# Optimization experiments

Measured on AMD Instinct MI355X. Metric: run time of the kernel, lower is better.

## Reference

```python
import jax, jax.numpy as jnp
import numpy as np

P = 50          # num_predicates
E = 2000        # num_entities
M = 64          # max_facts_per_query
F = 2_000_000   # num facts
N = 500_000     # num queries
BASE = E + 2    # pack base = max(constant_no, padding_idx) + 2


def setup_inputs() -> dict:
    key = jax.random.key(0)
    k1, k2, k3, k4, k5, k6 = jax.random.split(key, 6)
    fp = jax.random.randint(k1, (F,), 0, P, dtype=jnp.int32)
    fs = jax.random.randint(k2, (F,), 0, E, dtype=jnp.int32)
    fo = jax.random.randint(k3, (F,), 0, E, dtype=jnp.int32)
    facts_idx = jnp.stack([fp, fs, fo], axis=1)  # [F, 3]
    preds = jax.random.randint(k4, (N,), 0, P, dtype=jnp.int32)
    bound_args = jax.random.randint(k5, (N,), 0, E, dtype=jnp.int32)
    direction = jax.random.randint(k6, (N,), 0, 2, dtype=jnp.int32)
    return {"facts_idx": facts_idx, "preds": preds,
            "bound_args": bound_args, "direction": direction}


def _build_csr(keys, vals, num_buckets):
    """Sort vals by key; build offset table via scatter-add + cumsum (as in torch)."""
    order = jnp.argsort(keys)               # stable sort, matches pre-hash-sorted facts
    sorted_vals = vals[order]
    counts = jnp.zeros(num_buckets + 1, dtype=jnp.int32).at[keys + 1].add(1)
    offsets = jnp.cumsum(counts)
    return sorted_vals, offsets


def reference(facts_idx, preds, bound_args, direction):
    # --- _FactIndexBase: sort facts by packed 64-bit hash (lexicographic p,s,o) ---
    fp, fs, fo = facts_idx[:, 0], facts_idx[:, 1], facts_idx[:, 2]
    hashes = (fp * BASE + fs) * BASE + fo   # fits int32 for these dims
    h_order = jnp.argsort(hashes)
    fp, fs, fo = fp[h_order], fs[h_order], fo[h_order]

    # --- _build_inverted_indices: (pred,subj)->objs and (pred,obj)->subjs CSR ---
    ps_sorted_objs, ps_offsets = _build_csr(fp * E + fs, fo, P * E)
    po_sorted_subjs, po_offsets = _build_csr(fp * E + fo, fs, P * E)

    # --- enumerate() ---
    keys = preds * E + bound_args                               # [N]
    starts_ps = ps_offsets[keys]
    counts_ps = jnp.clip(ps_offsets[keys + 1] - starts_ps, 0, M)
    starts_po = po_offsets[keys]
    counts_po = jnp.clip(po_offsets[keys + 1] - starts_po, 0, M)
    is_obj = direction == 0                                     # [N] bool
    starts = jnp.where(is_obj, starts_ps, starts_po)
    counts = jnp.where(is_obj, counts_ps, counts_po)

    pos = jnp.arange(M, dtype=jnp.int32)[None, :]               # [1, M]
    valid = pos < counts[:, None]                               # [N, M]
    size = ps_sorted_objs.shape[0]                              # == F for both arrays
    gi = jnp.clip(starts[:, None] + pos, 0, size - 1)           # [N, M]
    vals_obj = ps_sorted_objs[gi]
    vals_subj = po_sorted_subjs[gi]
    candidates = jnp.where(is_obj[:, None], vals_obj, vals_subj)
    return candidates, valid
```

## Files before the change

### kernel.cpp

```cpp
#include <hip/hip_runtime.h>

#define PCONST 50
#define ECONST 2000
#define MCONST 64
#define NKEY   (PCONST * ECONST)
#define KPB    256
#define NBIN   ((NKEY + KPB - 1) / KPB)
#define NBIN2  (2 * NBIN)
#define SC_THREADS 1024
#define SC_CHUNK   8192
#define FPT    (SC_CHUNK / SC_THREADS)
#define CAP    6144

typedef int ivec4 __attribute__((ext_vector_type(4)));
typedef ivec4 ivec4_a4 __attribute__((aligned(4)));

__global__ void __launch_bounds__(SC_THREADS)
scatter_sort(const int* __restrict__ facts,
             int* __restrict__ bincur,
             unsigned* __restrict__ slab, int F) {
    __shared__ unsigned ordered[2 * SC_CHUNK];
    __shared__ int cnt[NBIN2];
    __shared__ int lbase[NBIN2];
    __shared__ int cur[NBIN2];
    __shared__ int base[NBIN2];
    __shared__ int wsum[16];

    int t = threadIdx.x;
    int blockStart = blockIdx.x * SC_CHUNK;
    int n = min(SC_CHUNK, F - blockStart);
    if (n <= 0) return;

    for (int i = t; i < NBIN2; i += SC_THREADS) cnt[i] = 0;
    __syncthreads();

    int myBase = blockStart + t * FPT;
    int myN = F - myBase;
    myN = (myN < 0) ? 0 : ((myN > FPT) ? FPT : myN);

    unsigned vps[FPT], vpo[FPT];

    if (myN == FPT) {
        const int4* p = (const int4*)(facts + 3 * myBase);
        int4 w0 = p[0], w1 = p[1], w2 = p[2], w3 = p[3], w4 = p[4], w5 = p[5];
        int kps, kpo;
        kps = w0.x * ECONST + w0.y; kpo = w0.x * ECONST + w0.z;
        vps[0] = ((unsigned)kps << 11) | (unsigned)w0.z;
        vpo[0] = ((unsigned)kpo << 11) | (unsigned)w0.y;
        atomicAdd(&cnt[kps >> 8], 1); atomicAdd(&cnt[NBIN + (kpo >> 8)], 1);
        kps = w0.w * ECONST + w1.x; kpo = w0.w * ECONST + w1.y;
        vps[1] = ((unsigned)kps << 11) | (unsigned)w1.y;
        vpo[1] = ((unsigned)kpo << 11) | (unsigned)w1.x;
        atomicAdd(&cnt[kps >> 8], 1); atomicAdd(&cnt[NBIN + (kpo >> 8)], 1);
        kps = w1.z * ECONST + w1.w; kpo = w1.z * ECONST + w2.x;
        vps[2] = ((unsigned)kps << 11) | (unsigned)w2.x;
        vpo[2] = ((unsigned)kpo << 11) | (unsigned)w1.w;
        atomicAdd(&cnt[kps >> 8], 1); atomicAdd(&cnt[NBIN + (kpo >> 8)], 1);
        kps = w2.y * ECONST + w2.z; kpo = w2.y * ECONST + w2.w;
        vps[3] = ((unsigned)kps << 11) | (unsigned)w2.w;
        vpo[3] = ((unsigned)kpo << 11) | (unsigned)w2.z;
        atomicAdd(&cnt[kps >> 8], 1); atomicAdd(&cnt[NBIN + (kpo >> 8)], 1);
        kps = w3.x * ECONST + w3.y; kpo = w3.x * ECONST + w3.z;
        vps[4] = ((unsigned)kps << 11) | (unsigned)w3.z;
        vpo[4] = ((unsigned)kpo << 11) | (unsigned)w3.y;
        atomicAdd(&cnt[kps >> 8], 1); atomicAdd(&cnt[NBIN + (kpo >> 8)], 1);
        kps = w3.w * ECONST + w4.x; kpo = w3.w * ECONST + w4.y;
        vps[5] = ((unsigned)kps << 11) | (unsigned)w4.y;
        vpo[5] = ((unsigned)kpo << 11) | (unsigned)w4.x;
        atomicAdd(&cnt[kps >> 8], 1); atomicAdd(&cnt[NBIN + (kpo >> 8)], 1);
        kps = w4.z * ECONST + w4.w; kpo = w4.z * ECONST + w5.x;
        vps[6] = ((unsigned)kps << 11) | (unsigned)w5.x;
        vpo[6] = ((unsigned)kpo << 11) | (unsigned)w4.w;
        atomicAdd(&cnt[kps >> 8], 1); atomicAdd(&cnt[NBIN + (kpo >> 8)], 1);
        kps = w5.y * ECONST + w5.z; kpo = w5.y * ECONST + w5.w;
        vps[7] = ((unsigned)kps << 11) | (unsigned)w5.w;
        vpo[7] = ((unsigned)kpo << 11) | (unsigned)w5.z;
        atomicAdd(&cnt[kps >> 8], 1); atomicAdd(&cnt[NBIN + (kpo >> 8)], 1);
    } else {
        for (int i = 0; i < myN; ++i) {
            int g = myBase + i;
            int fp = facts[3 * g], fs = facts[3 * g + 1], fo = facts[3 * g + 2];
            int kps = fp * ECONST + fs;
            int kpo = fp * ECONST + fo;
            vps[i] = ((unsigned)kps << 11) | (unsigned)fo;
            vpo[i] = ((unsigned)kpo << 11) | (unsigned)fs;
            atomicAdd(&cnt[kps >> 8], 1);
            atomicAdd(&cnt[NBIN + (kpo >> 8)], 1);
        }
    }
    __syncthreads();

    {
        int lane = t & 63, w = t >> 6;
        int c = (t < NBIN2) ? cnt[t] : 0;
        int inc = c;
        for (int d = 1; d < 64; d <<= 1) {
            int v = __shfl_up(inc, d);
            if (lane >= d) inc += v;
        }
        if (lane == 63) wsum[w] = inc;
        __syncthreads();
        if (t < NBIN2) {
            int wbase = 0;
            for (int i = 0; i < w; ++i) wbase += wsum[i];
            int excl = wbase + inc - c;
            lbase[t] = excl;
            cur[t]   = excl;
        }
    }
    __syncthreads();
    for (int i = t; i < NBIN2; i += SC_THREADS) {
        int c = cnt[i];
        base[i] = c ? atomicAdd(&bincur[i], c) : 0;
    }
    __syncthreads();

    #pragma unroll
    for (int i = 0; i < FPT; ++i) {
        if (i >= myN) break;
        unsigned ps = vps[i];
        int pos = atomicAdd(&cur[ps >> 19], 1);
        ordered[pos] = ps;
        unsigned po = vpo[i];
        pos = atomicAdd(&cur[NBIN + (po >> 19)], 1);
        ordered[pos] = (1u << 28) | po;
    }
    __syncthreads();

    int n2 = 2 * n;
    for (int j = t; j < n2; j += SC_THREADS) {
        unsigned v = ordered[j];
        int cbin = (int)((v >> 19) & 511u) + ((v >> 28) ? NBIN : 0);
        int pos  = base[cbin] + (j - lbase[cbin]);
        if (pos < CAP) slab[(size_t)cbin * CAP + pos] = v & 0x0FFFFFFFu;
    }
}

__global__ void binsort_kernel(const int* __restrict__ bincur,
                               const unsigned* __restrict__ slab,
                               int* __restrict__ off_ps,
                               int* __restrict__ off_po,
                               int* __restrict__ data_ps,
                               int* __restrict__ data_po, int F) {
    __shared__ unsigned buf[CAP];
    __shared__ unsigned short outv[CAP];
    __shared__ int hist[KPB];
    __shared__ int wsum[4];
    __shared__ int red[4];

    int wg = blockIdx.x;
    int* offout;
    int* data;
    const int* curbase;
    int b;
    if (wg < NBIN) { offout = off_ps; data = data_ps; curbase = bincur;        b = wg; }
    else           { offout = off_po; data = data_po; curbase = bincur + NBIN; b = wg - NBIN; }
    int t = threadIdx.x;
    int lane = t & 63, w = t >> 6;

    int s = 0;
    for (int i = t; i < b; i += KPB) s += curbase[i];
    for (int d = 1; d < 64; d <<= 1) s += __shfl_xor(s, d);
    if (lane == 0) red[w] = s;
    __syncthreads();
    int start = red[0] + red[1] + red[2] + red[3];

    int key0 = b * KPB;
    int len  = min(curbase[b], CAP);
    const unsigned* src = slab + (size_t)wg * CAP;

    if (t == 0 && b == 0) offout[NKEY] = F;

    for (int i = t; i < len; i += KPB) buf[i] = src[i];
    hist[t] = 0;
    __syncthreads();
    for (int i = t; i < len; i += KPB)
        atomicAdd(&hist[(int)(buf[i] >> 11) - key0], 1);
    __syncthreads();

    int c = hist[t];
    int inc = c;
    for (int d = 1; d < 64; d <<= 1) {
        int v = __shfl_up(inc, d);
        if (lane >= d) inc += v;
    }
    if (lane == 63) wsum[w] = inc;
    __syncthreads();
    int wbase = 0;
    for (int i = 0; i < w; ++i) wbase += wsum[i];
    int excl = wbase + inc - c;
    int gk = key0 + t;
    if (gk < NKEY) offout[gk] = start + excl;
    __syncthreads();
    hist[t] = excl;
    __syncthreads();

    for (int i = t; i < len; i += KPB) {
        unsigned v = buf[i];
        int lk  = (int)(v >> 11) - key0;
        int pos = atomicAdd(&hist[lk], 1);
        outv[pos] = (unsigned short)(v & 2047u);
    }
    __syncthreads();

    {
        int s0 = (t == 0) ? 0 : hist[t - 1];
        int e0 = hist[t];
        for (int i = s0 + 1; i < e0; ++i) {
            unsigned short v = outv[i]; int j = i - 1;
            while (j >= s0 && outv[j] > v) { outv[j + 1] = outv[j]; --j; }
            outv[j + 1] = v;
        }
    }
    __syncthreads();

    for (int i = t; i < len; i += KPB) data[start + i] = (int)outv[i];

    if ((wg == NBIN - 1 || wg == NBIN2 - 1) && t < 64 && len > 0)
        data[F + t] = (int)outv[len - 1];
}

__global__ void query_kernel(const int* __restrict__ preds,
                             const int* __restrict__ bound,
                             const int* __restrict__ dir,
                             const int* __restrict__ off_ps,
                             const int* __restrict__ off_po,
                             const int* __restrict__ vals_ps,
                             const int* __restrict__ vals_po,
                             int* __restrict__ cand,
                             int* __restrict__ valid, int N, int F) {
    int gwave  = (blockIdx.x * blockDim.x + threadIdx.x) >> 6;
    int lane   = threadIdx.x & 63;
    int nwaves = (gridDim.x * blockDim.x) >> 6;
    int grp = lane >> 4;
    int sl  = (lane & 15) * 4;

    for (int qb = gwave * 64; qb < N; qb += nwaves * 64) {
        int q = qb + lane;
        unsigned pk = 0;
        if (q < N) {
            int key = preds[q] * ECONST + bound[q];
            int dd  = dir[q];
            const int* off = (dd == 0) ? off_ps : off_po;
            int s0 = off[key];
            int c0 = min(off[key + 1] - s0, MCONST);
            if (c0 < 0) c0 = 0;
            pk = ((unsigned)s0 << 9) | ((unsigned)(dd != 0) << 8) | (unsigned)c0;
        }
        int nq = min(64, N - qb);
        for (int j4 = 0; j4 < nq; j4 += 4) {
            int j = j4 + grp;
            unsigned pj = (unsigned)__shfl((int)pk, j);
            if (j < nq) {
                int c  = (int)(pj & 255u);
                int s  = (int)(pj >> 9);
                const int* vals = (pj & 256u) ? vals_po : vals_ps;
                ivec4 cv = *(const ivec4_a4*)(vals + s + sl);
                ivec4 vv;
                vv.x = (sl     < c) ? 1 : 0;
                vv.y = (sl + 1 < c) ? 1 : 0;
                vv.z = (sl + 2 < c) ? 1 : 0;
                vv.w = (sl + 3 < c) ? 1 : 0;
                size_t o = (size_t)(qb + j) * MCONST + sl;
                __builtin_nontemporal_store(cv, (ivec4*)&cand[o]);
                __builtin_nontemporal_store(vv, (ivec4*)&valid[o]);
            }
        }
    }
}

extern "C" void kernel_launch(void* const* d_in, const int* in_sizes, int n_in,
                              void* d_out, int out_size, void* d_ws, size_t ws_size,
                              hipStream_t stream) {
    const int* facts = (const int*)d_in[0];
    const int* preds = (const int*)d_in[1];
    const int* bound = (const int*)d_in[2];
    const int* dir   = (const int*)d_in[3];
    int F = in_sizes[0] / 3;
    int N = in_sizes[1];

    int* ws       = (int*)d_ws;
    int* off_ps   = ws;
    int* off_po   = off_ps + NKEY + 4;
    int* bincur   = off_po + NKEY + 4;
    int* pad      = bincur + NBIN2;
    size_t ofs = (size_t)(pad - ws);
    ofs = (ofs + 3) & ~(size_t)3;
    int* data_ps = ws + ofs;
    int* data_po = data_ps + F + 64;
    unsigned* slab = (unsigned*)(data_po + F + 64);

    hipMemsetAsync(bincur, 0, (size_t)NBIN2 * sizeof(int), stream);

    int nChunks = (F + SC_CHUNK - 1) / SC_CHUNK;
    scatter_sort<<<nChunks, SC_THREADS, 0, stream>>>(facts, bincur, slab, F);
    binsort_kernel<<<NBIN2, KPB, 0, stream>>>(bincur, slab,
                                              off_ps, off_po, data_ps, data_po, F);

    int* cand  = (int*)d_out;
    int* valid = cand + (size_t)N * MCONST;
    int qBlocks = (N / 64 + 3) / 4 + 1;
    query_kernel<<<qBlocks, 256, 0, stream>>>(
        preds, bound, dir, off_ps, off_po, data_ps, data_po, cand, valid, N, F);
}
```

Measured before the change: 161.9 us.

## Pack start/count into one query table and store CSR values as 16-bit

The binsort kernel now writes a single packed table entry per key, holding the start offset shifted left 7 bits and the count clamped to 64. It no longer writes separate offset arrays for the two CSRs. Both CSR value arrays go into one shared ushort buffer, which halves the footprint of the gathered candidates. Each query then needs one table load instead of two offset loads, and reads 2-byte values. The cost is four scalar ushort loads per lane in place of one vector load. The packing assumes start offsets fit in 25 bits, which holds for 2F+64 at these sizes.

```diff
diff --git a/kernel.cpp b/kernel.cpp
--- a/kernel.cpp
+++ b/kernel.cpp
@@ -13,7 +13,6 @@
 #define CAP    6144
 
 typedef int ivec4 __attribute__((ext_vector_type(4)));
-typedef ivec4 ivec4_a4 __attribute__((aligned(4)));
 
 __global__ void __launch_bounds__(SC_THREADS)
 scatter_sort(const int* __restrict__ facts,
@@ -138,10 +137,9 @@
 
 __global__ void binsort_kernel(const int* __restrict__ bincur,
                                const unsigned* __restrict__ slab,
-                               int* __restrict__ off_ps,
-                               int* __restrict__ off_po,
-                               int* __restrict__ data_ps,
-                               int* __restrict__ data_po, int F) {
+                               unsigned* __restrict__ qtab,
+                               unsigned short* __restrict__ dataA,
+                               int F) {
     __shared__ unsigned buf[CAP];
     __shared__ unsigned short outv[CAP];
     __shared__ int hist[KPB];
@@ -149,12 +147,10 @@
     __shared__ int red[4];
 
     int wg = blockIdx.x;
-    int* offout;
-    int* data;
-    const int* curbase;
-    int b;
-    if (wg < NBIN) { offout = off_ps; data = data_ps; curbase = bincur;        b = wg; }
-    else           { offout = off_po; data = data_po; curbase = bincur + NBIN; b = wg - NBIN; }
+    int csr = (wg < NBIN) ? 0 : 1;
+    int b   = wg - csr * NBIN;
+    const int* curbase = bincur + csr * NBIN;
+    int gofs = csr ? (F + 64) : 0;
     int t = threadIdx.x;
     int lane = t & 63, w = t >> 6;
 
@@ -168,8 +164,6 @@
     int key0 = b * KPB;
     int len  = min(curbase[b], CAP);
     const unsigned* src = slab + (size_t)wg * CAP;
-
-    if (t == 0 && b == 0) offout[NKEY] = F;
 
     for (int i = t; i < len; i += KPB) buf[i] = src[i];
     hist[t] = 0;
@@ -190,7 +184,9 @@
     for (int i = 0; i < w; ++i) wbase += wsum[i];
     int excl = wbase + inc - c;
     int gk = key0 + t;
-    if (gk < NKEY) offout[gk] = start + excl;
+    if (gk < NKEY)
+        qtab[csr * NKEY + gk] =
+            ((unsigned)(gofs + start + excl) << 7) | (unsigned)min(c, MCONST);
     __syncthreads();
     hist[t] = excl;
     __syncthreads();
@@ -214,21 +210,19 @@
     }
     __syncthreads();
 
-    for (int i = t; i < len; i += KPB) data[start + i] = (int)outv[i];
+    for (int i = t; i < len; i += KPB) dataA[gofs + start + i] = outv[i];
 
     if ((wg == NBIN - 1 || wg == NBIN2 - 1) && t < 64 && len > 0)
-        data[F + t] = (int)outv[len - 1];
+        dataA[gofs + F + t] = outv[len - 1];
 }
 
 __global__ void query_kernel(const int* __restrict__ preds,
                              const int* __restrict__ bound,
                              const int* __restrict__ dir,
-                             const int* __restrict__ off_ps,
-                             const int* __restrict__ off_po,
-                             const int* __restrict__ vals_ps,
-                             const int* __restrict__ vals_po,
+                             const unsigned* __restrict__ qtab,
+                             const unsigned short* __restrict__ dataA,
                              int* __restrict__ cand,
-                             int* __restrict__ valid, int N, int F) {
+                             int* __restrict__ valid, int N) {
     int gwave  = (blockIdx.x * blockDim.x + threadIdx.x) >> 6;
     int lane   = threadIdx.x & 63;
     int nwaves = (gridDim.x * blockDim.x) >> 6;
@@ -239,24 +233,21 @@
         int q = qb + lane;
         unsigned pk = 0;
         if (q < N) {
-            int key = preds[q] * ECONST + bound[q];
-            int dd  = dir[q];
-            const int* off = (dd == 0) ? off_ps : off_po;
-            int s0 = off[key];
-            int c0 = min(off[key + 1] - s0, MCONST);
-            if (c0 < 0) c0 = 0;
-            pk = ((unsigned)s0 << 9) | ((unsigned)(dd != 0) << 8) | (unsigned)c0;
+            int idx = ((dir[q] != 0) ? NKEY : 0) + preds[q] * ECONST + bound[q];
+            pk = qtab[idx];
         }
         int nq = min(64, N - qb);
         for (int j4 = 0; j4 < nq; j4 += 4) {
             int j = j4 + grp;
             unsigned pj = (unsigned)__shfl((int)pk, j);
             if (j < nq) {
-                int c  = (int)(pj & 255u);
-                int s  = (int)(pj >> 9);
-                const int* vals = (pj & 256u) ? vals_po : vals_ps;
-                ivec4 cv = *(const ivec4_a4*)(vals + s + sl);
-                ivec4 vv;
+                int c = (int)(pj & 127u);
+                int s = (int)(pj >> 7);
+                ivec4 cv, vv;
+                cv.x = (int)dataA[s + sl];
+                cv.y = (int)dataA[s + sl + 1];
+                cv.z = (int)dataA[s + sl + 2];
+                cv.w = (int)dataA[s + sl + 3];
                 vv.x = (sl     < c) ? 1 : 0;
                 vv.y = (sl + 1 < c) ? 1 : 0;
                 vv.z = (sl + 2 < c) ? 1 : 0;
@@ -279,27 +270,24 @@
     int F = in_sizes[0] / 3;
     int N = in_sizes[1];
 
-    int* ws       = (int*)d_ws;
-    int* off_ps   = ws;
-    int* off_po   = off_ps + NKEY + 4;
-    int* bincur   = off_po + NKEY + 4;
-    int* pad      = bincur + NBIN2;
+    int* ws        = (int*)d_ws;
+    unsigned* qtab = (unsigned*)ws;
+    int* bincur    = ws + 2 * NKEY;
+    int* pad       = bincur + NBIN2;
     size_t ofs = (size_t)(pad - ws);
     ofs = (ofs + 3) & ~(size_t)3;
-    int* data_ps = ws + ofs;
-    int* data_po = data_ps + F + 64;
-    unsigned* slab = (unsigned*)(data_po + F + 64);
+    unsigned short* dataA = (unsigned short*)(ws + ofs);
+    unsigned* slab = (unsigned*)(dataA + 2 * (size_t)F + 128);
 
     hipMemsetAsync(bincur, 0, (size_t)NBIN2 * sizeof(int), stream);
 
     int nChunks = (F + SC_CHUNK - 1) / SC_CHUNK;
     scatter_sort<<<nChunks, SC_THREADS, 0, stream>>>(facts, bincur, slab, F);
-    binsort_kernel<<<NBIN2, KPB, 0, stream>>>(bincur, slab,
-                                              off_ps, off_po, data_ps, data_po, F);
+    binsort_kernel<<<NBIN2, KPB, 0, stream>>>(bincur, slab, qtab, dataA, F);
 
     int* cand  = (int*)d_out;
     int* valid = cand + (size_t)N * MCONST;
     int qBlocks = (N / 64 + 3) / 4 + 1;
     query_kernel<<<qBlocks, 256, 0, stream>>>(
-        preds, bound, dir, off_ps, off_po, data_ps, data_po, cand, valid, N, F);
-}
+        preds, bound, dir, qtab, dataA, cand, valid, N);
+}
```

After: 154.2 us. -4.7%, faster.
